# Kernel tuning notes

Hardware: AMD Instinct MI355X
Metric: run time of the kernel (lower is better)

## Reference

```python
import jax, jax.numpy as jnp
import numpy as np

V, E, H, L, T, B = 10000, 512, 1024, 2, 128, 64


def setup_inputs() -> dict:
    key = jax.random.key(0)
    ks = jax.random.split(key, 40)
    d = {}
    d["inputs"] = jax.random.randint(ks[0], (T, B), 0, V)
    d["hidden"] = jnp.zeros((L, B, H), jnp.float32)
    d["emb"] = jax.random.uniform(ks[1], (V, E), minval=-0.1, maxval=0.1)
    k = float(1.0 / np.sqrt(H))
    i = 2
    for l in range(L):
        isz = E if l == 0 else H
        for nm, bn in (("Wr", "br"), ("Wz", "bz"), ("Wh", "bh")):
            d[f"{nm}{l}"] = jax.random.uniform(ks[i], (H, isz), minval=-k, maxval=k); i += 1
            d[f"{bn}{l}"] = jax.random.uniform(ks[i], (H,), minval=-k, maxval=k); i += 1
        for nm in ("Ur", "Uz", "Uh"):
            d[f"{nm}{l}"] = jax.random.uniform(ks[i], (H, H), minval=-k, maxval=k); i += 1
    d["Wout"] = jax.random.uniform(ks[i], (V, H), minval=-0.1, maxval=0.1)
    d["bout"] = jnp.zeros((V,), jnp.float32)
    return d


def _gru_cell(x, h, Wr, br, Wz, bz, Wh, bh, Ur, Uz, Uh):
    # dropout is identity (dp_keep_prob=1.0)
    r = jax.nn.sigmoid(x @ Wr.T + br + h @ Ur.T)
    z = jax.nn.sigmoid(x @ Wz.T + bz + h @ Uz.T)
    h_tilde = jnp.tanh(x @ Wh.T + bh + (r * h) @ Uh.T)
    return (1.0 - z) * h + z * h_tilde


def reference(inputs, hidden, emb,
              Wr0, br0, Wz0, bz0, Wh0, bh0, Ur0, Uz0, Uh0,
              Wr1, br1, Wz1, bz1, Wh1, bh1, Ur1, Uz1, Uh1,
              Wout, bout):
    params = [
        (Wr0, br0, Wz0, bz0, Wh0, bh0, Ur0, Uz0, Uh0),
        (Wr1, br1, Wz1, bz1, Wh1, bh1, Ur1, Uz1, Uh1),
    ]
    x_emb = emb[inputs]  # [T, B, E]

    def step(carry, x_t):
        hs = []
        inp = x_t
        for l in range(L):
            h_new = _gru_cell(inp, carry[l], *params[l])
            hs.append(h_new)
            inp = h_new
        return jnp.stack(hs), inp

    h_final, top = jax.lax.scan(step, hidden, x_emb)  # top: [T, B, H]
    logits = top @ Wout.T + bout  # [T, B, V]
    return logits, h_final
```

## Files before the change

### kernel.cpp

```cpp
#include <hip/hip_runtime.h>
#include <hip/hip_bf16.h>
#include <math.h>

#define V 10000
#define E 512
#define H 1024
#define T 128
#define B 64
#define NWG 256
#define LDK 1032
#define RHSLOTS 32

typedef __bf16 bf16x8 __attribute__((ext_vector_type(8)));
typedef float f32x4 __attribute__((ext_vector_type(4)));
typedef unsigned short ushort8 __attribute__((ext_vector_type(8)));

__device__ __forceinline__ void store_f32_sc(float* p, float v) {
    asm volatile("global_store_dword %0, %1, off sc0 sc1" :: "v"(p), "v"(v) : "memory");
}
__device__ __forceinline__ void store_u16_sc(unsigned short* p, unsigned v) {
    asm volatile("global_store_short %0, %1, off sc0 sc1" :: "v"(p), "v"(v) : "memory");
}
__device__ __forceinline__ int load_i32_sc(const int* p) {
    int r;
    asm volatile("global_load_dword %0, %1, off sc0 sc1\n\ts_waitcnt vmcnt(0)"
                 : "=v"(r) : "v"(p) : "memory");
    return r;
}

__device__ __forceinline__ void gridbar_grp(int* gcnt, int gen) {
    asm volatile("s_waitcnt vmcnt(0)" ::: "memory");
    __syncthreads();
    if (threadIdx.x == 0)
        __hip_atomic_fetch_add(gcnt + (blockIdx.x & 7) * 32, 1,
                               __ATOMIC_RELAXED, __HIP_MEMORY_SCOPE_AGENT);
    if (threadIdx.x < 8) {
        const int target = gen * 8;
        while (load_i32_sc(gcnt + threadIdx.x * 32) < target)
            __builtin_amdgcn_s_sleep(2);
    }
    __syncthreads();
}

__device__ inline void splitpack(float4 v, uint2& hi, uint2& lo) {
    unsigned u0 = __float_as_uint(v.x), u1 = __float_as_uint(v.y);
    unsigned u2 = __float_as_uint(v.z), u3 = __float_as_uint(v.w);
    hi.x = __builtin_amdgcn_perm(u1, u0, 0x07060302u);
    hi.y = __builtin_amdgcn_perm(u3, u2, 0x07060302u);
    float l0 = v.x - __uint_as_float(u0 & 0xFFFF0000u);
    float l1 = v.y - __uint_as_float(u1 & 0xFFFF0000u);
    float l2 = v.z - __uint_as_float(u2 & 0xFFFF0000u);
    float l3 = v.w - __uint_as_float(u3 & 0xFFFF0000u);
    lo.x = __builtin_amdgcn_perm(__float_as_uint(l1), __float_as_uint(l0), 0x07060302u);
    lo.y = __builtin_amdgcn_perm(__float_as_uint(l3), __float_as_uint(l2), 0x07060302u);
}
__device__ inline void split1(float f, unsigned& hi, unsigned& lo) {
    unsigned u = __float_as_uint(f);
    hi = u >> 16;
    float l = f - __uint_as_float(u & 0xFFFF0000u);
    lo = __float_as_uint(l) >> 16;
}

__device__ __forceinline__ bf16x8 ld8(const unsigned short* p) {
    return __builtin_bit_cast(bf16x8, *(const ushort8*)p);
}
__device__ __forceinline__ f32x4 mfma3(f32x4 acc, bf16x8 ah, bf16x8 al,
                                       bf16x8 bh, bf16x8 bl) {
    acc = __builtin_amdgcn_mfma_f32_16x16x32_bf16(ah, bh, acc, 0, 0, 0);
    acc = __builtin_amdgcn_mfma_f32_16x16x32_bf16(al, bh, acc, 0, 0, 0);
    acc = __builtin_amdgcn_mfma_f32_16x16x32_bf16(ah, bl, acc, 0, 0, 0);
    return acc;
}

struct SplitSeg { const float* src; unsigned short* hi; unsigned short* lo; unsigned end; };
struct SplitTab { SplitSeg s[14]; };

__global__ __launch_bounds__(256) void split_all(SplitTab tab) {
    unsigned idx = blockIdx.x * 256 + threadIdx.x;
    unsigned base = 0;
    #pragma unroll
    for (int i = 0; i < 14; ++i) {
        if (idx < tab.s[i].end) {
            unsigned off = idx - base;
            float4 v = ((const float4*)tab.s[i].src)[off];
            uint2 h, l;
            splitpack(v, h, l);
            ((uint2*)tab.s[i].hi)[off] = h;
            ((uint2*)tab.s[i].lo)[off] = l;
            return;
        }
        base = tab.s[i].end;
    }
}

__global__ __launch_bounds__(256) void gemm_wx3h(
    const float* __restrict__ Af32,
    const unsigned short* __restrict__ Ahi, const unsigned short* __restrict__ Alo,
    const unsigned short* __restrict__ Whi, const unsigned short* __restrict__ Wlo,
    const float* __restrict__ b0, const float* __restrict__ b1, const float* __restrict__ b2,
    float* __restrict__ C, const int* __restrict__ rowidx, int K)
{
    __shared__ __align__(16) unsigned short Ah[128 * 40];
    __shared__ __align__(16) unsigned short Al[128 * 40];
    __shared__ __align__(16) unsigned short Bh[128 * 40];
    __shared__ __align__(16) unsigned short Bl[128 * 40];

    const int z = blockIdx.z;
    const float* __restrict__ bias = (z == 0) ? b0 : (z == 1) ? b1 : b2;
    const size_t zo = (size_t)z * H * K;

    const int tid  = threadIdx.x;
    const int lane = tid & 63;
    const int wv   = tid >> 6;
    const int wm   = wv & 1, wn = wv >> 1;
    const int bn = blockIdx.x * 128;
    const int bm = blockIdx.y * 128;

    const float* apt[4];
    unsigned lofs4[4];
    if (Af32) {
        #pragma unroll
        for (int i = 0; i < 4; ++i) {
            int f4 = i * 256 + tid, r = f4 >> 3, kq = f4 & 7;
            int gm = bm + r;
            int ar = rowidx ? rowidx[gm] : gm;
            apt[i] = Af32 + (size_t)ar * K + kq * 4;
            lofs4[i] = r * 40 + kq * 4;
        }
    }

    f32x4 acc[4][4];
    #pragma unroll
    for (int i = 0; i < 4; ++i)
        #pragma unroll
        for (int j = 0; j < 4; ++j) acc[i][j] = (f32x4){0.f, 0.f, 0.f, 0.f};

    const int la  = lane & 15;
    const int kg8 = (lane >> 4) * 8;

    for (int k0 = 0; k0 < K; k0 += 32) {
        __syncthreads();
        if (Af32) {
            #pragma unroll
            for (int i = 0; i < 4; ++i) {
                float4 va = *(const float4*)(apt[i] + k0);
                uint2 h, l;
                splitpack(va, h, l);
                *(uint2*)&Ah[lofs4[i]] = h;
                *(uint2*)&Al[lofs4[i]] = l;
            }
        } else {
            #pragma unroll
            for (int i = 0; i < 2; ++i) {
                int u8 = i * 256 + tid, r = u8 >> 2, c = (u8 & 3) * 8;
                *(ushort8*)&Ah[r * 40 + c] = *(const ushort8*)(Ahi + (size_t)(bm + r) * K + k0 + c);
                *(ushort8*)&Al[r * 40 + c] = *(const ushort8*)(Alo + (size_t)(bm + r) * K + k0 + c);
            }
        }
        #pragma unroll
        for (int i = 0; i < 2; ++i) {
            int u8 = i * 256 + tid, r = u8 >> 2, c = (u8 & 3) * 8;
            *(ushort8*)&Bh[r * 40 + c] = *(const ushort8*)(Whi + zo + (size_t)(bn + r) * K + k0 + c);
            *(ushort8*)&Bl[r * 40 + c] = *(const ushort8*)(Wlo + zo + (size_t)(bn + r) * K + k0 + c);
        }
        __syncthreads();

        bf16x8 ah[4], al[4];
        #pragma unroll
        for (int mt = 0; mt < 4; ++mt) {
            int row = (wm * 64 + mt * 16 + la) * 40 + kg8;
            ah[mt] = ld8(&Ah[row]);
            al[mt] = ld8(&Al[row]);
        }
        #pragma unroll
        for (int nt = 0; nt < 4; ++nt) {
            int row = (wn * 64 + nt * 16 + la) * 40 + kg8;
            bf16x8 bh = ld8(&Bh[row]);
            bf16x8 bl = ld8(&Bl[row]);
            #pragma unroll
            for (int mt = 0; mt < 4; ++mt)
                acc[mt][nt] = mfma3(acc[mt][nt], ah[mt], al[mt], bh, bl);
        }
    }

    #pragma unroll
    for (int mt = 0; mt < 4; ++mt) {
        int mrow = bm + wm * 64 + mt * 16 + (lane >> 4) * 4;
        #pragma unroll
        for (int nt = 0; nt < 4; ++nt) {
            int n = bn + wn * 64 + nt * 16 + la;
            float bi = bias[n];
            #pragma unroll
            for (int r = 0; r < 4; ++r)
                C[(size_t)(mrow + r) * (3 * H) + n + z * H] = acc[mt][nt][r] + bi;
        }
    }
}

__global__ __launch_bounds__(256) void gemm_logits(
    const unsigned short* __restrict__ Ahi, const unsigned short* __restrict__ Alo,
    const unsigned short* __restrict__ Bhi, const unsigned short* __restrict__ Blo,
    const float* __restrict__ bias, float* __restrict__ C, int N, int K)
{
    __shared__ __align__(16) unsigned short Ah[128 * 40];
    __shared__ __align__(16) unsigned short Al[128 * 40];
    __shared__ __align__(16) unsigned short Bh[128 * 40];
    __shared__ __align__(16) unsigned short Bl[128 * 40];

    const int tid  = threadIdx.x;
    const int lane = tid & 63;
    const int wv   = tid >> 6;
    const int wm   = wv & 1, wn = wv >> 1;
    const int bn = blockIdx.x * 128;
    const int bm = blockIdx.y * 128;

    f32x4 acc[4][4];
    #pragma unroll
    for (int i = 0; i < 4; ++i)
        #pragma unroll
        for (int j = 0; j < 4; ++j) acc[i][j] = (f32x4){0.f, 0.f, 0.f, 0.f};

    const int la  = lane & 15;
    const int kg8 = (lane >> 4) * 8;

    for (int k0 = 0; k0 < K; k0 += 32) {
        __syncthreads();
        #pragma unroll
        for (int i = 0; i < 2; ++i) {
            int u8 = i * 256 + tid, r = u8 >> 2, c = (u8 & 3) * 8;
            *(ushort8*)&Ah[r * 40 + c] = *(const ushort8*)(Ahi + (size_t)(bm + r) * K + k0 + c);
            *(ushort8*)&Al[r * 40 + c] = *(const ushort8*)(Alo + (size_t)(bm + r) * K + k0 + c);
            int brow = bn + r;
            int br = (brow < N) ? brow : 0;
            *(ushort8*)&Bh[r * 40 + c] = *(const ushort8*)(Bhi + (size_t)br * K + k0 + c);
            *(ushort8*)&Bl[r * 40 + c] = *(const ushort8*)(Blo + (size_t)br * K + k0 + c);
        }
        __syncthreads();

        bf16x8 ah[4], al[4];
        #pragma unroll
        for (int mt = 0; mt < 4; ++mt) {
            int row = (wm * 64 + mt * 16 + la) * 40 + kg8;
            ah[mt] = ld8(&Ah[row]);
            al[mt] = ld8(&Al[row]);
        }
        #pragma unroll
        for (int nt = 0; nt < 4; ++nt) {
            int row = (wn * 64 + nt * 16 + la) * 40 + kg8;
            bf16x8 bh = ld8(&Bh[row]);
            bf16x8 bl = ld8(&Bl[row]);
            #pragma unroll
            for (int mt = 0; mt < 4; ++mt)
                acc[mt][nt] = mfma3(acc[mt][nt], ah[mt], al[mt], bh, bl);
        }
    }

    #pragma unroll
    for (int mt = 0; mt < 4; ++mt) {
        int mrow = bm + wm * 64 + mt * 16 + (lane >> 4) * 4;
        #pragma unroll
        for (int nt = 0; nt < 4; ++nt) {
            int n = bn + wn * 64 + nt * 16 + la;
            if (n < N) {
                float bi = bias[n];
                #pragma unroll
                for (int r = 0; r < 4; ++r)
                    C[(size_t)(mrow + r) * N + n] = acc[mt][nt][r] + bi;
            }
        }
    }
}

__global__ __launch_bounds__(1024, 1) void gru_layer(
    const unsigned short* __restrict__ Uhi, const unsigned short* __restrict__ Ulo,
    const float* __restrict__ Wx, const float* __restrict__ hinit,
    const unsigned short* __restrict__ hstg_hi, const unsigned short* __restrict__ hstg_lo,
    unsigned short* __restrict__ h_hi, unsigned short* __restrict__ h_lo,
    unsigned short* __restrict__ rh_hi, unsigned short* __restrict__ rh_lo,
    float* __restrict__ hfin, int* cnt)
{
    extern __shared__ char smem[];
    unsigned short* hs_hi = (unsigned short*)smem;
    unsigned short* hs_lo = hs_hi + 16 * LDK;
    f32x4* red = (f32x4*)(hs_lo + 16 * LDK);

    const int tid  = threadIdx.x;
    const int lane = tid & 63;
    const int kh   = __builtin_amdgcn_readfirstlane(tid >> 6);
    const int la   = lane & 15;
    const int kg8  = (lane >> 4) * 8;
    const int erow = (lane >> 4) * 4;

    const int bid = blockIdx.x;
    const int xcd = bid & 7;
    const int sub = bid >> 3;
    const int grp = sub & 3;
    const int m0  = grp * 16;
    const int j0  = (xcd * 8 + (sub >> 2)) * 16;
    int* gcnt = cnt + grp * 8 * 32;

    const size_t HH = (size_t)H * H;
    const unsigned short* Ur_hi = Uhi;
    const unsigned short* Uz_hi = Uhi + HH;
    const unsigned short* Uh_hi = Uhi + 2 * HH;
    const unsigned short* Ur_lo = Ulo;
    const unsigned short* Uz_lo = Ulo + HH;
    const unsigned short* Uh_lo = Ulo + 2 * HH;

    int gen = 0;
    const int rbase = m0 + erow;

    f32x4 zreg = (f32x4){0.f, 0.f, 0.f, 0.f};
    float hvC[4] = {0.f, 0.f, 0.f, 0.f};
    float wrC[4], wzC[4], whC[4];
    float wrN[4], wzN[4], whN[4];
    if (kh == 0) {
        #pragma unroll
        for (int qq = 0; qq < 4; ++qq) {
            hvC[qq] = hinit[(size_t)(rbase + qq) * H + j0 + la];
            const size_t wb = ((size_t)0 * B + rbase + qq) * (3 * H) + j0 + la;
            wrC[qq] = Wx[wb];
            wzC[qq] = Wx[wb + H];
            whC[qq] = Wx[wb + 2 * H];
        }
    }

    for (int t = 0; t < T; ++t) {
        const size_t rbs = (size_t)(t & (RHSLOTS - 1)) * B * H;

        {
            const unsigned short* ph = (t == 0) ? hstg_hi : (h_hi + (size_t)(t - 1) * B * H);
            const unsigned short* pl = (t == 0) ? hstg_lo : (h_lo + (size_t)(t - 1) * B * H);
            #pragma unroll
            for (int j = 0; j < 2; ++j) {
                int u8 = j * 1024 + tid;
                int r = u8 >> 7, c = (u8 & 127) * 8;
                *(ushort8*)&hs_hi[r * LDK + c] = *(const ushort8*)(ph + (size_t)(m0 + r) * H + c);
                *(ushort8*)&hs_lo[r * LDK + c] = *(const ushort8*)(pl + (size_t)(m0 + r) * H + c);
            }
            __syncthreads();
            f32x4 a0 = (f32x4){0.f, 0.f, 0.f, 0.f}, a1 = a0;
            const int kb = kh * 64 + kg8;
            #pragma unroll
            for (int ks = 0; ks < 2; ++ks) {
                const int ko = kb + ks * 32;
                const int ar = la * LDK + ko;
                bf16x8 ah = ld8(&hs_hi[ar]);
                bf16x8 al = ld8(&hs_lo[ar]);
                const size_t ub = (size_t)(j0 + la) * H + ko;
                a0 = mfma3(a0, ah, al, ld8(Ur_hi + ub), ld8(Ur_lo + ub));
                a1 = mfma3(a1, ah, al, ld8(Uz_hi + ub), ld8(Uz_lo + ub));
            }
            if (kh) {
                red[((kh - 1) * 2 + 0) * 64 + lane] = a0;
                red[((kh - 1) * 2 + 1) * 64 + lane] = a1;
            }
            __syncthreads();
            if (kh == 0) {
                #pragma unroll
                for (int w = 0; w < 15; ++w) {
                    a0 += red[(w * 2 + 0) * 64 + lane];
                    a1 += red[(w * 2 + 1) * 64 + lane];
                }
                #pragma unroll
                for (int qq = 0; qq < 4; ++qq) {
                    float rg = 1.f / (1.f + __expf(-(a0[qq] + wrC[qq])));
                    zreg[qq] = 1.f / (1.f + __expf(-(a1[qq] + wzC[qq])));
                    float rh = rg * hvC[qq];
                    unsigned rhh, rhl;
                    split1(rh, rhh, rhl);
                    const size_t ix = rbs + (size_t)(rbase + qq) * H + j0 + la;
                    store_u16_sc(rh_hi + ix, rhh);
                    store_u16_sc(rh_lo + ix, rhl);
                }
            }
        }
        gridbar_grp(gcnt, ++gen);

        {
            if (kh == 0 && t + 1 < T) {
                #pragma unroll
                for (int qq = 0; qq < 4; ++qq) {
                    const size_t wb = ((size_t)(t + 1) * B + rbase + qq) * (3 * H) + j0 + la;
                    wrN[qq] = Wx[wb];
                    wzN[qq] = Wx[wb + H];
                    whN[qq] = Wx[wb + 2 * H];
                }
            }
            #pragma unroll
            for (int j = 0; j < 2; ++j) {
                int u8 = j * 1024 + tid;
                int r = u8 >> 7, c = (u8 & 127) * 8;
                *(ushort8*)&hs_hi[r * LDK + c] = *(const ushort8*)(rh_hi + rbs + (size_t)(m0 + r) * H + c);
                *(ushort8*)&hs_lo[r * LDK + c] = *(const ushort8*)(rh_lo + rbs + (size_t)(m0 + r) * H + c);
            }
            __syncthreads();
            f32x4 a = (f32x4){0.f, 0.f, 0.f, 0.f};
            const int kb = kh * 64 + kg8;
            #pragma unroll
            for (int ks = 0; ks < 2; ++ks) {
                const int ko = kb + ks * 32;
                const int ar = la * LDK + ko;
                const size_t ub = (size_t)(j0 + la) * H + ko;
                a = mfma3(a, ld8(&hs_hi[ar]), ld8(&hs_lo[ar]),
                          ld8(Uh_hi + ub), ld8(Uh_lo + ub));
            }
            if (kh) red[(kh - 1) * 64 + lane] = a;
            __syncthreads();
            if (kh == 0) {
                #pragma unroll
                for (int w = 0; w < 15; ++w) a += red[w * 64 + lane];
                #pragma unroll
                for (int qq = 0; qq < 4; ++qq) {
                    float ht = tanhf(a[qq] + whC[qq]);
                    float hn = (1.f - zreg[qq]) * hvC[qq] + zreg[qq] * ht;
                    unsigned hh, hl;
                    split1(hn, hh, hl);
                    const size_t ix = (size_t)t * B * H + (size_t)(rbase + qq) * H + j0 + la;
                    store_u16_sc(h_hi + ix, hh);
                    store_u16_sc(h_lo + ix, hl);
                    if (t == T - 1)
                        store_f32_sc(hfin + (size_t)(rbase + qq) * H + j0 + la, hn);
                    hvC[qq] = hn;
                    wrC[qq] = wrN[qq];
                    wzC[qq] = wzN[qq];
                    whC[qq] = whN[qq];
                }
            }
        }
        gridbar_grp(gcnt, ++gen);
    }
}

extern "C" void kernel_launch(void* const* d_in, const int* in_sizes, int n_in,
                              void* d_out, int out_size, void* d_ws, size_t ws_size,
                              hipStream_t stream)
{
    const int*   tok    = (const int*)d_in[0];
    const float* hidden = (const float*)d_in[1];
    const float* emb    = (const float*)d_in[2];
    const float* Wr0 = (const float*)d_in[3],  *br0 = (const float*)d_in[4];
    const float* Wz0 = (const float*)d_in[5],  *bz0 = (const float*)d_in[6];
    const float* Wh0 = (const float*)d_in[7],  *bh0 = (const float*)d_in[8];
    const float* Ur0 = (const float*)d_in[9],  *Uz0 = (const float*)d_in[10], *Uh0 = (const float*)d_in[11];
    const float* Wr1 = (const float*)d_in[12], *br1 = (const float*)d_in[13];
    const float* Wz1 = (const float*)d_in[14], *bz1 = (const float*)d_in[15];
    const float* Wh1 = (const float*)d_in[16], *bh1 = (const float*)d_in[17];
    const float* Ur1 = (const float*)d_in[18], *Uz1 = (const float*)d_in[19], *Uh1 = (const float*)d_in[20];
    const float* Wout = (const float*)d_in[21], *bout = (const float*)d_in[22];
    float* out = (float*)d_out;

    const size_t HH = (size_t)H * H;
    const size_t HE = (size_t)H * E;
    const size_t TBH = (size_t)T * B * H;
    const size_t VH = (size_t)V * H;

    float* ws = (float*)d_ws;
    float* Wx = ws;
    unsigned short* u16 = (unsigned short*)(Wx + 3 * TBH);
    unsigned short* U0hi = u16;            u16 += 3 * HH;
    unsigned short* U0lo = u16;            u16 += 3 * HH;
    unsigned short* U1hi = u16;            u16 += 3 * HH;
    unsigned short* U1lo = u16;            u16 += 3 * HH;
    unsigned short* W1hi = u16;            u16 += 3 * HH;
    unsigned short* W1lo = u16;            u16 += 3 * HH;
    unsigned short* W0hi = u16;            u16 += 3 * HE;
    unsigned short* W0lo = u16;            u16 += 3 * HE;
    unsigned short* Wouthi = u16;          u16 += VH;
    unsigned short* Woutlo = u16;          u16 += VH;
    unsigned short* hidhi = u16;           u16 += 2 * (size_t)B * H;
    unsigned short* hidlo = u16;           u16 += 2 * (size_t)B * H;
    unsigned short* h0hi = u16;            u16 += TBH;
    unsigned short* h0lo = u16;            u16 += TBH;
    unsigned short* h1hi = u16;            u16 += TBH;
    unsigned short* h1lo = u16;            u16 += TBH;
    unsigned short* rh0hi = u16;           u16 += (size_t)RHSLOTS * B * H;
    unsigned short* rh0lo = u16;           u16 += (size_t)RHSLOTS * B * H;
    unsigned short* rh1hi = u16;           u16 += (size_t)RHSLOTS * B * H;
    unsigned short* rh1lo = u16;           u16 += (size_t)RHSLOTS * B * H;
    int* cnt0 = (int*)u16;
    int* cnt1 = cnt0 + 4 * 8 * 32;

    static bool attr_set = false;
    if (!attr_set) {
        (void)hipFuncSetAttribute((const void*)gru_layer,
                                  hipFuncAttributeMaxDynamicSharedMemorySize, 96768);
        attr_set = true;
    }

    (void)hipMemsetAsync(cnt0, 0, 2 * 4 * 8 * 32 * sizeof(int), stream);

    const unsigned nU = (unsigned)(HH / 4), nW0 = (unsigned)(HE / 4);
    const unsigned nWout = (unsigned)(VH / 4), nHid = (unsigned)(2 * B * H / 4);
    SplitTab tab;
    unsigned acc = 0;
    const float* srcs[14] = {Ur0, Uz0, Uh0, Ur1, Uz1, Uh1, Wr1, Wz1, Wh1,
                             Wr0, Wz0, Wh0, Wout, hidden};
    unsigned short* his[14] = {U0hi, U0hi + HH, U0hi + 2 * HH, U1hi, U1hi + HH, U1hi + 2 * HH,
                               W1hi, W1hi + HH, W1hi + 2 * HH,
                               W0hi, W0hi + HE, W0hi + 2 * HE, Wouthi, hidhi};
    unsigned short* los[14] = {U0lo, U0lo + HH, U0lo + 2 * HH, U1lo, U1lo + HH, U1lo + 2 * HH,
                               W1lo, W1lo + HH, W1lo + 2 * HH,
                               W0lo, W0lo + HE, W0lo + 2 * HE, Woutlo, hidlo};
    unsigned cnts[14] = {nU, nU, nU, nU, nU, nU, nU, nU, nU, nW0, nW0, nW0, nWout, nHid};
    for (int i = 0; i < 14; ++i) {
        acc += cnts[i];
        tab.s[i] = {srcs[i], his[i], los[i], acc};
    }
    split_all<<<acc / 256, 256, 0, stream>>>(tab);

    gemm_wx3h<<<dim3(H / 128, T * B / 128, 3), 256, 0, stream>>>(
        emb, nullptr, nullptr, W0hi, W0lo, br0, bz0, bh0, Wx, tok, E);

    gru_layer<<<NWG, 1024, 96768, stream>>>(
        U0hi, U0lo, Wx, hidden, hidhi, hidlo,
        h0hi, h0lo, rh0hi, rh0lo, out + (size_t)T * B * V, cnt0);

    gemm_wx3h<<<dim3(H / 128, T * B / 128, 3), 256, 0, stream>>>(
        nullptr, h0hi, h0lo, W1hi, W1lo, br1, bz1, bh1, Wx, nullptr, H);

    gru_layer<<<NWG, 1024, 96768, stream>>>(
        U1hi, U1lo, Wx, hidden + (size_t)B * H, hidhi + (size_t)B * H, hidlo + (size_t)B * H,
        h1hi, h1lo, rh1hi, rh1lo, out + (size_t)T * B * V + (size_t)B * H, cnt1);

    gemm_logits<<<dim3((V + 127) / 128, T * B / 128), 256, 0, stream>>>(
        h1hi, h1lo, Wouthi, Woutlo, bout, out, V, H);
}
```

Measured before the change: 3.723 ms.

## Store GRU hidden states as fp32 and split to bf16 hi/lo at load

Result: faster. 3.498 ms (-6.0%).

```diff
diff --git a/kernel.cpp b/kernel.cpp
--- a/kernel.cpp
+++ b/kernel.cpp
@@ -9,7 +9,6 @@
 #define B 64
 #define NWG 256
 #define LDK 1032
-#define RHSLOTS 32
 
 typedef __bf16 bf16x8 __attribute__((ext_vector_type(8)));
 typedef float f32x4 __attribute__((ext_vector_type(4)));
@@ -17,9 +16,6 @@
 
 __device__ __forceinline__ void store_f32_sc(float* p, float v) {
     asm volatile("global_store_dword %0, %1, off sc0 sc1" :: "v"(p), "v"(v) : "memory");
-}
-__device__ __forceinline__ void store_u16_sc(unsigned short* p, unsigned v) {
-    asm volatile("global_store_short %0, %1, off sc0 sc1" :: "v"(p), "v"(v) : "memory");
 }
 __device__ __forceinline__ int load_i32_sc(const int* p) {
     int r;
@@ -54,12 +50,6 @@
     lo.x = __builtin_amdgcn_perm(__float_as_uint(l1), __float_as_uint(l0), 0x07060302u);
     lo.y = __builtin_amdgcn_perm(__float_as_uint(l3), __float_as_uint(l2), 0x07060302u);
 }
-__device__ inline void split1(float f, unsigned& hi, unsigned& lo) {
-    unsigned u = __float_as_uint(f);
-    hi = u >> 16;
-    float l = f - __uint_as_float(u & 0xFFFF0000u);
-    lo = __float_as_uint(l) >> 16;
-}
 
 __device__ __forceinline__ bf16x8 ld8(const unsigned short* p) {
     return __builtin_bit_cast(bf16x8, *(const ushort8*)p);
@@ -73,13 +63,13 @@
 }
 
 struct SplitSeg { const float* src; unsigned short* hi; unsigned short* lo; unsigned end; };
-struct SplitTab { SplitSeg s[14]; };
+struct SplitTab { SplitSeg s[13]; };
 
 __global__ __launch_bounds__(256) void split_all(SplitTab tab) {
     unsigned idx = blockIdx.x * 256 + threadIdx.x;
     unsigned base = 0;
     #pragma unroll
-    for (int i = 0; i < 14; ++i) {
+    for (int i = 0; i < 13; ++i) {
         if (idx < tab.s[i].end) {
             unsigned off = idx - base;
             float4 v = ((const float4*)tab.s[i].src)[off];
@@ -94,8 +84,7 @@
 }
 
 __global__ __launch_bounds__(256) void gemm_wx3h(
-    const float* __restrict__ Af32,
-    const unsigned short* __restrict__ Ahi, const unsigned short* __restrict__ Alo,
+    const float* __restrict__ A,
     const unsigned short* __restrict__ Whi, const unsigned short* __restrict__ Wlo,
     const float* __restrict__ b0, const float* __restrict__ b1, const float* __restrict__ b2,
     float* __restrict__ C, const int* __restrict__ rowidx, int K)
@@ -118,15 +107,13 @@
 
     const float* apt[4];
     unsigned lofs4[4];
-    if (Af32) {
-        #pragma unroll
-        for (int i = 0; i < 4; ++i) {
-            int f4 = i * 256 + tid, r = f4 >> 3, kq = f4 & 7;
-            int gm = bm + r;
-            int ar = rowidx ? rowidx[gm] : gm;
-            apt[i] = Af32 + (size_t)ar * K + kq * 4;
-            lofs4[i] = r * 40 + kq * 4;
-        }
+    #pragma unroll
+    for (int i = 0; i < 4; ++i) {
+        int f4 = i * 256 + tid, r = f4 >> 3, kq = f4 & 7;
+        int gm = bm + r;
+        int ar = rowidx ? rowidx[gm] : gm;
+        apt[i] = A + (size_t)ar * K + kq * 4;
+        lofs4[i] = r * 40 + kq * 4;
     }
 
     f32x4 acc[4][4];
@@ -140,22 +127,13 @@
 
     for (int k0 = 0; k0 < K; k0 += 32) {
         __syncthreads();
-        if (Af32) {
-            #pragma unroll
-            for (int i = 0; i < 4; ++i) {
-                float4 va = *(const float4*)(apt[i] + k0);
-                uint2 h, l;
-                splitpack(va, h, l);
-                *(uint2*)&Ah[lofs4[i]] = h;
-                *(uint2*)&Al[lofs4[i]] = l;
-            }
-        } else {
-            #pragma unroll
-            for (int i = 0; i < 2; ++i) {
-                int u8 = i * 256 + tid, r = u8 >> 2, c = (u8 & 3) * 8;
-                *(ushort8*)&Ah[r * 40 + c] = *(const ushort8*)(Ahi + (size_t)(bm + r) * K + k0 + c);
-                *(ushort8*)&Al[r * 40 + c] = *(const ushort8*)(Alo + (size_t)(bm + r) * K + k0 + c);
-            }
+        #pragma unroll
+        for (int i = 0; i < 4; ++i) {
+            float4 va = *(const float4*)(apt[i] + k0);
+            uint2 h, l;
+            splitpack(va, h, l);
+            *(uint2*)&Ah[lofs4[i]] = h;
+            *(uint2*)&Al[lofs4[i]] = l;
         }
         #pragma unroll
         for (int i = 0; i < 2; ++i) {
@@ -198,7 +176,7 @@
 }
 
 __global__ __launch_bounds__(256) void gemm_logits(
-    const unsigned short* __restrict__ Ahi, const unsigned short* __restrict__ Alo,
+    const float* __restrict__ A,
     const unsigned short* __restrict__ Bhi, const unsigned short* __restrict__ Blo,
     const float* __restrict__ bias, float* __restrict__ C, int N, int K)
 {
@@ -214,6 +192,15 @@
     const int bn = blockIdx.x * 128;
     const int bm = blockIdx.y * 128;
 
+    const float* apt[4];
+    unsigned lofs4[4];
+    #pragma unroll
+    for (int i = 0; i < 4; ++i) {
+        int f4 = i * 256 + tid, r = f4 >> 3, kq = f4 & 7;
+        apt[i] = A + (size_t)(bm + r) * K + kq * 4;
+        lofs4[i] = r * 40 + kq * 4;
+    }
+
     f32x4 acc[4][4];
     #pragma unroll
     for (int i = 0; i < 4; ++i)
@@ -226,10 +213,16 @@
     for (int k0 = 0; k0 < K; k0 += 32) {
         __syncthreads();
         #pragma unroll
+        for (int i = 0; i < 4; ++i) {
+            float4 va = *(const float4*)(apt[i] + k0);
+            uint2 h, l;
+            splitpack(va, h, l);
+            *(uint2*)&Ah[lofs4[i]] = h;
+            *(uint2*)&Al[lofs4[i]] = l;
+        }
+        #pragma unroll
         for (int i = 0; i < 2; ++i) {
             int u8 = i * 256 + tid, r = u8 >> 2, c = (u8 & 3) * 8;
-            *(ushort8*)&Ah[r * 40 + c] = *(const ushort8*)(Ahi + (size_t)(bm + r) * K + k0 + c);
-            *(ushort8*)&Al[r * 40 + c] = *(const ushort8*)(Alo + (size_t)(bm + r) * K + k0 + c);
             int brow = bn + r;
             int br = (brow < N) ? brow : 0;
             *(ushort8*)&Bh[r * 40 + c] = *(const ushort8*)(Bhi + (size_t)br * K + k0 + c);
@@ -274,9 +267,7 @@
 __global__ __launch_bounds__(1024, 1) void gru_layer(
     const unsigned short* __restrict__ Uhi, const unsigned short* __restrict__ Ulo,
     const float* __restrict__ Wx, const float* __restrict__ hinit,
-    const unsigned short* __restrict__ hstg_hi, const unsigned short* __restrict__ hstg_lo,
-    unsigned short* __restrict__ h_hi, unsigned short* __restrict__ h_lo,
-    unsigned short* __restrict__ rh_hi, unsigned short* __restrict__ rh_lo,
+    float* __restrict__ hRM, float* __restrict__ rhRM,
     float* __restrict__ hfin, int* cnt)
 {
     extern __shared__ char smem[];
@@ -290,6 +281,8 @@
     const int la   = lane & 15;
     const int kg8  = (lane >> 4) * 8;
     const int erow = (lane >> 4) * 4;
+    const int trow = tid >> 6;
+    const int tq   = tid & 63;
 
     const int bid = blockIdx.x;
     const int xcd = bid & 7;
@@ -326,17 +319,20 @@
     }
 
     for (int t = 0; t < T; ++t) {
-        const size_t rbs = (size_t)(t & (RHSLOTS - 1)) * B * H;
+        const float* hprev = (t == 0) ? hinit : (hRM + (size_t)(t - 1) * B * H);
 
         {
-            const unsigned short* ph = (t == 0) ? hstg_hi : (h_hi + (size_t)(t - 1) * B * H);
-            const unsigned short* pl = (t == 0) ? hstg_lo : (h_lo + (size_t)(t - 1) * B * H);
-            #pragma unroll
-            for (int j = 0; j < 2; ++j) {
-                int u8 = j * 1024 + tid;
-                int r = u8 >> 7, c = (u8 & 127) * 8;
-                *(ushort8*)&hs_hi[r * LDK + c] = *(const ushort8*)(ph + (size_t)(m0 + r) * H + c);
-                *(ushort8*)&hs_lo[r * LDK + c] = *(const ushort8*)(pl + (size_t)(m0 + r) * H + c);
+            {
+                const float* hrp = hprev + (size_t)(m0 + trow) * H;
+                #pragma unroll
+                for (int i = 0; i < 4; ++i) {
+                    const int c = (tq + i * 64) * 4;
+                    float4 v = *(const float4*)(hrp + c);
+                    uint2 h2, l2;
+                    splitpack(v, h2, l2);
+                    *(uint2*)&hs_hi[trow * LDK + c] = h2;
+                    *(uint2*)&hs_lo[trow * LDK + c] = l2;
+                }
             }
             __syncthreads();
             f32x4 a0 = (f32x4){0.f, 0.f, 0.f, 0.f}, a1 = a0;
@@ -366,12 +362,8 @@
                 for (int qq = 0; qq < 4; ++qq) {
                     float rg = 1.f / (1.f + __expf(-(a0[qq] + wrC[qq])));
                     zreg[qq] = 1.f / (1.f + __expf(-(a1[qq] + wzC[qq])));
-                    float rh = rg * hvC[qq];
-                    unsigned rhh, rhl;
-                    split1(rh, rhh, rhl);
-                    const size_t ix = rbs + (size_t)(rbase + qq) * H + j0 + la;
-                    store_u16_sc(rh_hi + ix, rhh);
-                    store_u16_sc(rh_lo + ix, rhl);
+                    store_f32_sc(rhRM + ((size_t)t * B + rbase + qq) * H + j0 + la,
+                                 rg * hvC[qq]);
                 }
             }
         }
@@ -387,12 +379,17 @@
                     whN[qq] = Wx[wb + 2 * H];
                 }
             }
-            #pragma unroll
-            for (int j = 0; j < 2; ++j) {
-                int u8 = j * 1024 + tid;
-                int r = u8 >> 7, c = (u8 & 127) * 8;
-                *(ushort8*)&hs_hi[r * LDK + c] = *(const ushort8*)(rh_hi + rbs + (size_t)(m0 + r) * H + c);
-                *(ushort8*)&hs_lo[r * LDK + c] = *(const ushort8*)(rh_lo + rbs + (size_t)(m0 + r) * H + c);
+            {
+                const float* rrp = rhRM + (size_t)t * B * H + (size_t)(m0 + trow) * H;
+                #pragma unroll
+                for (int i = 0; i < 4; ++i) {
+                    const int c = (tq + i * 64) * 4;
+                    float4 v = *(const float4*)(rrp + c);
+                    uint2 h2, l2;
+                    splitpack(v, h2, l2);
+                    *(uint2*)&hs_hi[trow * LDK + c] = h2;
+                    *(uint2*)&hs_lo[trow * LDK + c] = l2;
+                }
             }
             __syncthreads();
             f32x4 a = (f32x4){0.f, 0.f, 0.f, 0.f};
@@ -414,11 +411,7 @@
                 for (int qq = 0; qq < 4; ++qq) {
                     float ht = tanhf(a[qq] + whC[qq]);
                     float hn = (1.f - zreg[qq]) * hvC[qq] + zreg[qq] * ht;
-                    unsigned hh, hl;
-                    split1(hn, hh, hl);
-                    const size_t ix = (size_t)t * B * H + (size_t)(rbase + qq) * H + j0 + la;
-                    store_u16_sc(h_hi + ix, hh);
-                    store_u16_sc(h_lo + ix, hl);
+                    store_f32_sc(hRM + ((size_t)t * B + rbase + qq) * H + j0 + la, hn);
                     if (t == T - 1)
                         store_f32_sc(hfin + (size_t)(rbase + qq) * H + j0 + la, hn);
                     hvC[qq] = hn;
@@ -456,28 +449,22 @@
     const size_t VH = (size_t)V * H;
 
     float* ws = (float*)d_ws;
-    float* Wx = ws;
-    unsigned short* u16 = (unsigned short*)(Wx + 3 * TBH);
-    unsigned short* U0hi = u16;            u16 += 3 * HH;
-    unsigned short* U0lo = u16;            u16 += 3 * HH;
-    unsigned short* U1hi = u16;            u16 += 3 * HH;
-    unsigned short* U1lo = u16;            u16 += 3 * HH;
-    unsigned short* W1hi = u16;            u16 += 3 * HH;
-    unsigned short* W1lo = u16;            u16 += 3 * HH;
-    unsigned short* W0hi = u16;            u16 += 3 * HE;
-    unsigned short* W0lo = u16;            u16 += 3 * HE;
-    unsigned short* Wouthi = u16;          u16 += VH;
-    unsigned short* Woutlo = u16;          u16 += VH;
-    unsigned short* hidhi = u16;           u16 += 2 * (size_t)B * H;
-    unsigned short* hidlo = u16;           u16 += 2 * (size_t)B * H;
-    unsigned short* h0hi = u16;            u16 += TBH;
-    unsigned short* h0lo = u16;            u16 += TBH;
-    unsigned short* h1hi = u16;            u16 += TBH;
-    unsigned short* h1lo = u16;            u16 += TBH;
-    unsigned short* rh0hi = u16;           u16 += (size_t)RHSLOTS * B * H;
-    unsigned short* rh0lo = u16;           u16 += (size_t)RHSLOTS * B * H;
-    unsigned short* rh1hi = u16;           u16 += (size_t)RHSLOTS * B * H;
-    unsigned short* rh1lo = u16;           u16 += (size_t)RHSLOTS * B * H;
+    float* Wx    = ws;
+    float* h0RM  = Wx    + 3 * TBH;
+    float* rh0RM = h0RM  + TBH;
+    float* h1RM  = rh0RM + TBH;
+    float* rh1RM = h1RM  + TBH;
+    unsigned short* u16 = (unsigned short*)(rh1RM + TBH);
+    unsigned short* U0hi = u16;    u16 += 3 * HH;
+    unsigned short* U0lo = u16;    u16 += 3 * HH;
+    unsigned short* U1hi = u16;    u16 += 3 * HH;
+    unsigned short* U1lo = u16;    u16 += 3 * HH;
+    unsigned short* W1hi = u16;    u16 += 3 * HH;
+    unsigned short* W1lo = u16;    u16 += 3 * HH;
+    unsigned short* W0hi = u16;    u16 += 3 * HE;
+    unsigned short* W0lo = u16;    u16 += 3 * HE;
+    unsigned short* Wouthi = u16;  u16 += VH;
+    unsigned short* Woutlo = u16;  u16 += VH;
     int* cnt0 = (int*)u16;
     int* cnt1 = cnt0 + 4 * 8 * 32;
 
@@ -491,38 +478,37 @@
     (void)hipMemsetAsync(cnt0, 0, 2 * 4 * 8 * 32 * sizeof(int), stream);
 
     const unsigned nU = (unsigned)(HH / 4), nW0 = (unsigned)(HE / 4);
-    const unsigned nWout = (unsigned)(VH / 4), nHid = (unsigned)(2 * B * H / 4);
+    const unsigned nWout = (unsigned)(VH / 4);
     SplitTab tab;
     unsigned acc = 0;
-    const float* srcs[14] = {Ur0, Uz0, Uh0, Ur1, Uz1, Uh1, Wr1, Wz1, Wh1,
-                             Wr0, Wz0, Wh0, Wout, hidden};
-    unsigned short* his[14] = {U0hi, U0hi + HH, U0hi + 2 * HH, U1hi, U1hi + HH, U1hi + 2 * HH,
+    const float* srcs[13] = {Ur0, Uz0, Uh0, Ur1, Uz1, Uh1, Wr1, Wz1, Wh1,
+                             Wr0, Wz0, Wh0, Wout};
+    unsigned short* his[13] = {U0hi, U0hi + HH, U0hi + 2 * HH, U1hi, U1hi + HH, U1hi + 2 * HH,
                                W1hi, W1hi + HH, W1hi + 2 * HH,
-                               W0hi, W0hi + HE, W0hi + 2 * HE, Wouthi, hidhi};
-    unsigned short* los[14] = {U0lo, U0lo + HH, U0lo + 2 * HH, U1lo, U1lo + HH, U1lo + 2 * HH,
+                               W0hi, W0hi + HE, W0hi + 2 * HE, Wouthi};
+    unsigned short* los[13] = {U0lo, U0lo + HH, U0lo + 2 * HH, U1lo, U1lo + HH, U1lo + 2 * HH,
                                W1lo, W1lo + HH, W1lo + 2 * HH,
-                               W0lo, W0lo + HE, W0lo + 2 * HE, Woutlo, hidlo};
-    unsigned cnts[14] = {nU, nU, nU, nU, nU, nU, nU, nU, nU, nW0, nW0, nW0, nWout, nHid};
-    for (int i = 0; i < 14; ++i) {
+                               W0lo, W0lo + HE, W0lo + 2 * HE, Woutlo};
+    unsigned cnts[13] = {nU, nU, nU, nU, nU, nU, nU, nU, nU, nW0, nW0, nW0, nWout};
+    for (int i = 0; i < 13; ++i) {
         acc += cnts[i];
         tab.s[i] = {srcs[i], his[i], los[i], acc};
     }
     split_all<<<acc / 256, 256, 0, stream>>>(tab);
 
     gemm_wx3h<<<dim3(H / 128, T * B / 128, 3), 256, 0, stream>>>(
-        emb, nullptr, nullptr, W0hi, W0lo, br0, bz0, bh0, Wx, tok, E);
-
-    gru_layer<<<NWG, 1024, 96768, stream>>>(
-        U0hi, U0lo, Wx, hidden, hidhi, hidlo,
-        h0hi, h0lo, rh0hi, rh0lo, out + (size_t)T * B * V, cnt0);
+        emb, W0hi, W0lo, br0, bz0, bh0, Wx, tok, E);
+
+    gru_layer<<<NWG, 1024, 96768, stream>>>(U0hi, U0lo, Wx, hidden,
+                                            h0RM, rh0RM, out + (size_t)T * B * V, cnt0);
 
     gemm_wx3h<<<dim3(H / 128, T * B / 128, 3), 256, 0, stream>>>(
-        nullptr, h0hi, h0lo, W1hi, W1lo, br1, bz1, bh1, Wx, nullptr, H);
-
-    gru_layer<<<NWG, 1024, 96768, stream>>>(
-        U1hi, U1lo, Wx, hidden + (size_t)B * H, hidhi + (size_t)B * H, hidlo + (size_t)B * H,
-        h1hi, h1lo, rh1hi, rh1lo, out + (size_t)T * B * V + (size_t)B * H, cnt1);
+        h0RM, W1hi, W1lo, br1, bz1, bh1, Wx, nullptr, H);
+
+    gru_layer<<<NWG, 1024, 96768, stream>>>(U1hi, U1lo, Wx, hidden + (size_t)B * H,
+                                            h1RM, rh1RM,
+                                            out + (size_t)T * B * V + (size_t)B * H, cnt1);
 
     gemm_logits<<<dim3((V + 127) / 128, T * B / 128), 256, 0, stream>>>(
-        h1hi, h1lo, Wouthi, Woutlo, bout, out, V, H);
-}
+        h1RM, Wouthi, Woutlo, bout, out, V, H);
+}
```
